# Performance work log

Hardware: AMD Instinct MI355X
Metric: run time of the kernel (lower is better)

Reference implementation:

```python
import jax, jax.numpy as jnp
import numpy as np

E, T, H, I, K = 32, 2048, 1024, 512, 4


def setup_inputs() -> dict:
    key = jax.random.key(0)
    k1, k2, k3, k4, k5 = jax.random.split(key, 5)
    hidden_states = jax.random.normal(k1, (T, H), dtype=jnp.float32)
    top_k_index = jax.random.randint(k2, (T, K), 0, E)
    w = jax.random.uniform(k3, (T, K), dtype=jnp.float32)
    top_k_weights = w / jnp.sum(w, axis=-1, keepdims=True)  # router-like normalized weights
    gate_up_proj = jax.random.normal(k4, (E, 2 * I, H), dtype=jnp.float32) * 0.02
    down_proj = jax.random.normal(k5, (E, H, I), dtype=jnp.float32) * 0.02
    return {
        "hidden_states": hidden_states,
        "top_k_index": top_k_index,
        "top_k_weights": top_k_weights,
        "gate_up_proj": gate_up_proj,
        "down_proj": down_proj,
    }


def reference(hidden_states, top_k_index, top_k_weights, gate_up_proj, down_proj):
    # Faithful to the eager MoE dispatch loop: for each expert e, gather the
    # tokens routed to it, run gate/up/down SwiGLU, scale by routing weight,
    # and scatter-add into the output. Expressed as a scan over experts with a
    # per-token routing weight that is 0 for unrouted tokens (identical math:
    # index_add over (token, slot) pairs == sum_k where(idx==e, w, 0)).
    num_experts = gate_up_proj.shape[0]
    inter = down_proj.shape[2]

    def expert_step(acc, xs):
        gup_w, down_w, e = xs  # [2I, H], [H, I], scalar expert id
        # combined routing weight per token for this expert: [T]
        w_tok = jnp.sum(jnp.where(top_k_index == e, top_k_weights, 0.0), axis=1)
        gu = hidden_states @ gup_w.T              # [T, 2I]
        gate, up = gu[:, :inter], gu[:, inter:]
        h = jax.nn.silu(gate) * up                # [T, I]
        out = h @ down_w.T                        # [T, H]
        return acc + out * w_tok[:, None], None

    init = jnp.zeros_like(hidden_states)
    final_hidden_states, _ = jax.lax.scan(
        expert_step, init,
        (gate_up_proj, down_proj, jnp.arange(num_experts)),
    )
    return final_hidden_states
```

## Files before the change

### kernel.cpp

```cpp
#include <hip/hip_runtime.h>

#define NE 32
#define NT 2048
#define NH 1024
#define NI 512
#define NK 4
#define CAP 512

typedef __attribute__((ext_vector_type(8))) short short8;
typedef __attribute__((ext_vector_type(4))) float floatx4;

static __device__ __forceinline__ unsigned pk_bf16(float x, float y) {
#if __has_builtin(__builtin_amdgcn_cvt_pk_bf16_f32)
    typedef __attribute__((ext_vector_type(2))) __bf16 bf16x2;
    union { bf16x2 v; unsigned u; } c;
    c.v = __builtin_amdgcn_cvt_pk_bf16_f32(x, y);
    return c.u;
#else
    union { float f; unsigned u; } a, b;
    a.f = x; b.f = y;
    unsigned ua = (a.u + 0x7fffu + ((a.u >> 16) & 1u)) >> 16;
    unsigned ub = (b.u + 0x7fffu + ((b.u >> 16) & 1u)) >> 16;
    return (ua & 0xffffu) | (ub << 16);
#endif
}

static __device__ __forceinline__ short8 pack8(const float* p) {
    union { unsigned u[4]; short8 s; } c;
    c.u[0] = pk_bf16(p[0], p[1]);
    c.u[1] = pk_bf16(p[2], p[3]);
    c.u[2] = pk_bf16(p[4], p[5]);
    c.u[3] = pk_bf16(p[6], p[7]);
    return c.s;
}

static __device__ __forceinline__ unsigned short bf16_1(float x) {
    return (unsigned short)(pk_bf16(x, 0.f) & 0xffffu);
}

__global__ void route_kernel(const int* __restrict__ idx,
                             const float* __restrict__ w,
                             int* __restrict__ counts,
                             int* __restrict__ tok,
                             float* __restrict__ wgt) {
    int tid = blockIdx.x * blockDim.x + threadIdx.x;
    if (tid >= NT * NK) return;
    int e = idx[tid];
    int pos = atomicAdd(&counts[e], 1);
    if (pos < CAP) {
        tok[e * CAP + pos] = tid;
        wgt[e * CAP + pos] = w[tid];
    }
}

__global__ void cvt_hidden(const float* __restrict__ hidden,
                           unsigned short* __restrict__ hb16) {
    size_t i = (size_t)(blockIdx.x * 256 + threadIdx.x) * 8;
    float tmp[8];
    *(floatx4*)tmp       = *(const floatx4*)(hidden + i);
    *(floatx4*)(tmp + 4) = *(const floatx4*)(hidden + i + 4);
    *(short8*)(hb16 + i) = pack8(tmp);
}


__global__ __launch_bounds__(256, 2) void gateup_mfma(
    const unsigned short* __restrict__ hb16,
    const float* __restrict__ gup,
    const int* __restrict__ counts,
    const int* __restrict__ tok,
    unsigned short* __restrict__ hbuf)
{
    int e = blockIdx.z;
    int cnt = counts[e]; if (cnt > CAP) cnt = CAP;
    int m0 = blockIdx.y * 128;
    if (m0 >= cnt) return;
    int j0 = blockIdx.x * 64;

    __shared__ __align__(16) short As[2][128][64];
    __shared__ __align__(16) short Bs[2][128][64];

    int tid = threadIdx.x;
    int sr = tid >> 3;
    int sg = tid & 7;

    const unsigned short* aptr[4];
    short* awr[4];
    const float* bptr[4];
    short* bwr[4];
    const float* gup_e = gup + (size_t)e * (2 * NI) * NH;
#pragma unroll
    for (int p = 0; p < 4; p++) {
        int r = p * 32 + sr;
        int mi = m0 + r;
        int tk = tok[e * CAP + (mi < cnt ? mi : m0)];
        aptr[p] = hb16 + (size_t)(tk >> 2) * NH + sg * 8;
        awr[p]  = &As[0][r][(sg ^ (r & 7)) * 8];
        int gj = (r < 64) ? (j0 + r) : (NI + j0 + (r - 64));
        bptr[p] = gup_e + (size_t)gj * NH + sg * 8;
        bwr[p]  = &Bs[0][r][(sg ^ (r & 7)) * 8];
    }

    int wave = tid >> 6, lane = tid & 63;
    int wm = wave >> 1;
    int wj = wave & 1;
    int lcol = lane & 15;
    int quad = lane >> 4;

    floatx4 acc[4][4];
#pragma unroll
    for (int a = 0; a < 4; a++)
#pragma unroll
        for (int b = 0; b < 4; b++) acc[a][b] = (floatx4){0.f, 0.f, 0.f, 0.f};

    short8 ra[4];
    float4 rb[8];
#pragma unroll
    for (int p = 0; p < 4; p++) {
        ra[p] = *(const short8*)(aptr[p]);
        rb[2 * p]     = *(const float4*)(bptr[p]);
        rb[2 * p + 1] = *(const float4*)(bptr[p] + 4);
    }
#pragma unroll
    for (int p = 0; p < 4; p++) {
        *(short8*)(awr[p]) = ra[p];
        union { unsigned u[4]; short8 s; } c;
        c.u[0] = pk_bf16(rb[2 * p].x, rb[2 * p].y);
        c.u[1] = pk_bf16(rb[2 * p].z, rb[2 * p].w);
        c.u[2] = pk_bf16(rb[2 * p + 1].x, rb[2 * p + 1].y);
        c.u[3] = pk_bf16(rb[2 * p + 1].z, rb[2 * p + 1].w);
        *(short8*)(bwr[p]) = c.s;
    }
#pragma unroll
    for (int p = 0; p < 4; p++) {
        ra[p] = *(const short8*)(aptr[p] + 64);
        rb[2 * p]     = *(const float4*)(bptr[p] + 64);
        rb[2 * p + 1] = *(const float4*)(bptr[p] + 68);
    }
    __syncthreads();

    const int NIT = NH / 64;
    for (int it = 0; it < NIT; ++it) {
        int cur = it & 1;
        int co = cur * 8192;
#pragma unroll
        for (int ks = 0; ks < 2; ks++) {
            short8 af[4], bfr[4];
            int q = ks * 4 + quad;
#pragma unroll
            for (int mt = 0; mt < 4; mt++) {
                int R = wm * 64 + mt * 16 + lcol;
                af[mt] = *(const short8*)&As[cur][R][(q ^ (R & 7)) * 8];
            }
#pragma unroll
            for (int nt = 0; nt < 4; nt++) {
                int R = (nt < 2) ? (wj * 32 + nt * 16 + lcol)
                                 : (64 + wj * 32 + (nt - 2) * 16 + lcol);
                bfr[nt] = *(const short8*)&Bs[cur][R][(q ^ (R & 7)) * 8];
            }
#pragma unroll
            for (int mt = 0; mt < 4; mt++)
#pragma unroll
                for (int nt = 0; nt < 4; nt++)
                    acc[mt][nt] = __builtin_amdgcn_mfma_f32_16x16x32_bf16(
                        af[mt], bfr[nt], acc[mt][nt], 0, 0, 0);
        }
        if (it + 1 < NIT) {
            int no = (co ^ 8192);
#pragma unroll
            for (int p = 0; p < 4; p++) {
                *(short8*)(awr[p] + no) = ra[p];
                union { unsigned u[4]; short8 s; } c;
                c.u[0] = pk_bf16(rb[2 * p].x, rb[2 * p].y);
                c.u[1] = pk_bf16(rb[2 * p].z, rb[2 * p].w);
                c.u[2] = pk_bf16(rb[2 * p + 1].x, rb[2 * p + 1].y);
                c.u[3] = pk_bf16(rb[2 * p + 1].z, rb[2 * p + 1].w);
                *(short8*)(bwr[p] + no) = c.s;
            }
            if (it + 2 < NIT) {
                int h2 = (it + 2) * 64;
#pragma unroll
                for (int p = 0; p < 4; p++) {
                    ra[p] = *(const short8*)(aptr[p] + h2);
                    rb[2 * p]     = *(const float4*)(bptr[p] + h2);
                    rb[2 * p + 1] = *(const float4*)(bptr[p] + h2 + 4);
                }
            }
            __syncthreads();
        }
    }

#pragma unroll
    for (int mt = 0; mt < 4; mt++) {
#pragma unroll
        for (int i = 0; i < 4; i++) {
            int m = wm * 64 + mt * 16 + quad * 4 + i;
            if (m0 + m < cnt) {
                int tk = tok[e * CAP + m0 + m];
                unsigned short* hp = hbuf + (size_t)tk * NI + j0 + wj * 32 + lcol;
#pragma unroll
                for (int nt = 0; nt < 2; nt++) {
                    float g = acc[mt][nt][i];
                    float u = acc[mt][nt + 2][i];
                    float h = g / (1.f + __expf(-g)) * u;
                    hp[nt * 16] = bf16_1(h);
                }
            }
        }
    }
}

__global__ __launch_bounds__(256, 2) void down_mfma(
    const unsigned short* __restrict__ hbuf,
    const float* __restrict__ down,
    const int* __restrict__ counts,
    const int* __restrict__ tok,
    const float* __restrict__ wgt,
    float* __restrict__ out)
{
    int e = blockIdx.z;
    int cnt = counts[e]; if (cnt > CAP) cnt = CAP;
    int m0 = blockIdx.y * 128;
    if (m0 >= cnt) return;
    int n0 = blockIdx.x * 128;

    __shared__ __align__(16) short As[2][128][64];
    __shared__ __align__(16) short Bs[2][128][64];

    int tid = threadIdx.x;
    int sr = tid >> 3;
    int sg = tid & 7;

    const unsigned short* aptr[4];
    short* awr[4];
    const float* bptr[4];
    short* bwr[4];
    const float* down_e = down + (size_t)e * NH * NI;
#pragma unroll
    for (int p = 0; p < 4; p++) {
        int r = p * 32 + sr;
        int mi = m0 + r;
        int tk = tok[e * CAP + (mi < cnt ? mi : m0)];
        aptr[p] = hbuf + (size_t)tk * NI + sg * 8;
        awr[p]  = &As[0][r][(sg ^ (r & 7)) * 8];
        bptr[p] = down_e + (size_t)(n0 + r) * NI + sg * 8;
        bwr[p]  = &Bs[0][r][(sg ^ (r & 7)) * 8];
    }

    int wave = tid >> 6, lane = tid & 63;
    int wm = wave >> 1, wn = wave & 1;
    int lcol = lane & 15;
    int quad = lane >> 4;

    floatx4 acc[4][4];
#pragma unroll
    for (int a = 0; a < 4; a++)
#pragma unroll
        for (int b = 0; b < 4; b++) acc[a][b] = (floatx4){0.f, 0.f, 0.f, 0.f};

    short8 ra[4];
    float4 rb[8];
#pragma unroll
    for (int p = 0; p < 4; p++) {
        ra[p] = *(const short8*)(aptr[p]);
        rb[2 * p]     = *(const float4*)(bptr[p]);
        rb[2 * p + 1] = *(const float4*)(bptr[p] + 4);
    }
#pragma unroll
    for (int p = 0; p < 4; p++) {
        *(short8*)(awr[p]) = ra[p];
        union { unsigned u[4]; short8 s; } c;
        c.u[0] = pk_bf16(rb[2 * p].x, rb[2 * p].y);
        c.u[1] = pk_bf16(rb[2 * p].z, rb[2 * p].w);
        c.u[2] = pk_bf16(rb[2 * p + 1].x, rb[2 * p + 1].y);
        c.u[3] = pk_bf16(rb[2 * p + 1].z, rb[2 * p + 1].w);
        *(short8*)(bwr[p]) = c.s;
    }
#pragma unroll
    for (int p = 0; p < 4; p++) {
        ra[p] = *(const short8*)(aptr[p] + 64);
        rb[2 * p]     = *(const float4*)(bptr[p] + 64);
        rb[2 * p + 1] = *(const float4*)(bptr[p] + 68);
    }
    __syncthreads();

    const int NIT = NI / 64;
    for (int it = 0; it < NIT; ++it) {
        int cur = it & 1;
#pragma unroll
        for (int ks = 0; ks < 2; ks++) {
            short8 af[4], bfr[4];
            int q = ks * 4 + quad;
#pragma unroll
            for (int mt = 0; mt < 4; mt++) {
                int R = wm * 64 + mt * 16 + lcol;
                af[mt] = *(const short8*)&As[cur][R][(q ^ (R & 7)) * 8];
            }
#pragma unroll
            for (int nt = 0; nt < 4; nt++) {
                int R = wn * 64 + nt * 16 + lcol;
                bfr[nt] = *(const short8*)&Bs[cur][R][(q ^ (R & 7)) * 8];
            }
#pragma unroll
            for (int mt = 0; mt < 4; mt++)
#pragma unroll
                for (int nt = 0; nt < 4; nt++)
                    acc[mt][nt] = __builtin_amdgcn_mfma_f32_16x16x32_bf16(
                        af[mt], bfr[nt], acc[mt][nt], 0, 0, 0);
        }
        if (it + 1 < NIT) {
            int no = ((cur ^ 1)) * 8192;
#pragma unroll
            for (int p = 0; p < 4; p++) {
                *(short8*)(awr[p] + no) = ra[p];
                union { unsigned u[4]; short8 s; } c;
                c.u[0] = pk_bf16(rb[2 * p].x, rb[2 * p].y);
                c.u[1] = pk_bf16(rb[2 * p].z, rb[2 * p].w);
                c.u[2] = pk_bf16(rb[2 * p + 1].x, rb[2 * p + 1].y);
                c.u[3] = pk_bf16(rb[2 * p + 1].z, rb[2 * p + 1].w);
                *(short8*)(bwr[p] + no) = c.s;
            }
            if (it + 2 < NIT) {
                int i2 = (it + 2) * 64;
#pragma unroll
                for (int p = 0; p < 4; p++) {
                    ra[p] = *(const short8*)(aptr[p] + i2);
                    rb[2 * p]     = *(const float4*)(bptr[p] + i2);
                    rb[2 * p + 1] = *(const float4*)(bptr[p] + i2 + 4);
                }
            }
            __syncthreads();
        }
    }

#pragma unroll
    for (int mt = 0; mt < 4; mt++)
#pragma unroll
        for (int i = 0; i < 4; i++) {
            int m = wm * 64 + mt * 16 + quad * 4 + i;
            if (m0 + m < cnt) {
                int tk = tok[e * CAP + m0 + m];
                float wl = wgt[e * CAP + m0 + m];
                float* op = out + (size_t)(tk >> 2) * NH + n0 + wn * 64 + lcol;
#pragma unroll
                for (int nt = 0; nt < 4; nt++)
                    atomicAdd(op + nt * 16, acc[mt][nt][i] * wl);
            }
        }
}

extern "C" void kernel_launch(void* const* d_in, const int* in_sizes, int n_in,
                              void* d_out, int out_size, void* d_ws, size_t ws_size,
                              hipStream_t stream) {
    const float* hidden = (const float*)d_in[0];
    const int*   tk_idx = (const int*)d_in[1];
    const float* tk_w   = (const float*)d_in[2];
    const float* gup    = (const float*)d_in[3];
    const float* down   = (const float*)d_in[4];
    float* out = (float*)d_out;

    char* ws = (char*)d_ws;
    int*            counts = (int*)ws;
    int*            tok    = (int*)(ws + 256);
    float*          wgt    = (float*)(ws + 256 + NE * CAP * 4);
    unsigned short* hb16   = (unsigned short*)(ws + 256 + 2 * NE * CAP * 4);
    unsigned short* hbuf   = (unsigned short*)(ws + 256 + 2 * NE * CAP * 4
                                               + (size_t)NT * NH * 2);

    hipMemsetAsync(counts, 0, 256, stream);
    hipMemsetAsync(out, 0, (size_t)NT * NH * sizeof(float), stream);

    route_kernel<<<(NT * NK + 255) / 256, 256, 0, stream>>>(tk_idx, tk_w, counts, tok, wgt);
    cvt_hidden<<<(NT * NH / 8) / 256, 256, 0, stream>>>(hidden, hb16);

    dim3 gridG(NI / 64, CAP / 128, NE);
    gateup_mfma<<<gridG, 256, 0, stream>>>(hb16, gup, counts, tok, hbuf);

    dim3 gridD(NH / 128, CAP / 128, NE);
    down_mfma<<<gridD, 256, 0, stream>>>(hbuf, down, counts, tok, wgt, out);
}
```

Measured before the change: 346.0 us.

## Pre-convert expert weights to bf16 and single-buffer LDS tiles in GEMMs

Adds a generic bf16 conversion kernel that converts the gate/up and down weights, as well as the hidden states, into workspace buffers on every call. Both MFMA GEMM kernels then load bf16 weights directly with no per-tile conversion. Their LDS staging drops from double- to single-buffered, with an extra barrier per iteration, and the launch bound rises to 3 blocks per CU. The goal is to remove conversion work and register pressure from the GEMM inner loops and raise occupancy. The cost is a full extra read and write pass over roughly 192MB of fp32 weights per call, plus less overlap between loads and compute.

```diff
diff --git a/kernel.cpp b/kernel.cpp
--- a/kernel.cpp
+++ b/kernel.cpp
@@ -25,15 +25,6 @@
 #endif
 }
 
-static __device__ __forceinline__ short8 pack8(const float* p) {
-    union { unsigned u[4]; short8 s; } c;
-    c.u[0] = pk_bf16(p[0], p[1]);
-    c.u[1] = pk_bf16(p[2], p[3]);
-    c.u[2] = pk_bf16(p[4], p[5]);
-    c.u[3] = pk_bf16(p[6], p[7]);
-    return c.s;
-}
-
 static __device__ __forceinline__ unsigned short bf16_1(float x) {
     return (unsigned short)(pk_bf16(x, 0.f) & 0xffffu);
 }
@@ -53,19 +44,25 @@
     }
 }
 
-__global__ void cvt_hidden(const float* __restrict__ hidden,
-                           unsigned short* __restrict__ hb16) {
-    size_t i = (size_t)(blockIdx.x * 256 + threadIdx.x) * 8;
-    float tmp[8];
-    *(floatx4*)tmp       = *(const floatx4*)(hidden + i);
-    *(floatx4*)(tmp + 4) = *(const floatx4*)(hidden + i + 4);
-    *(short8*)(hb16 + i) = pack8(tmp);
-}
-
-
-__global__ __launch_bounds__(256, 2) void gateup_mfma(
+__global__ void cvt_bf16(const float* __restrict__ src,
+                         unsigned short* __restrict__ dst, int n8) {
+    int i = blockIdx.x * 256 + threadIdx.x;
+    if (i >= n8) return;
+    size_t o = (size_t)i * 8;
+    float4 a = *(const float4*)(src + o);
+    float4 b = *(const float4*)(src + o + 4);
+    union { unsigned u[4]; short8 s; } c;
+    c.u[0] = pk_bf16(a.x, a.y);
+    c.u[1] = pk_bf16(a.z, a.w);
+    c.u[2] = pk_bf16(b.x, b.y);
+    c.u[3] = pk_bf16(b.z, b.w);
+    *(short8*)(dst + o) = c.s;
+}
+
+
+__global__ __launch_bounds__(256, 3) void gateup_mfma(
     const unsigned short* __restrict__ hb16,
-    const float* __restrict__ gup,
+    const unsigned short* __restrict__ gupb,
     const int* __restrict__ counts,
     const int* __restrict__ tok,
     unsigned short* __restrict__ hbuf)
@@ -76,28 +73,28 @@
     if (m0 >= cnt) return;
     int j0 = blockIdx.x * 64;
 
-    __shared__ __align__(16) short As[2][128][64];
-    __shared__ __align__(16) short Bs[2][128][64];
+    __shared__ __align__(16) short As[128][64];
+    __shared__ __align__(16) short Bs[128][64];
 
     int tid = threadIdx.x;
     int sr = tid >> 3;
     int sg = tid & 7;
 
     const unsigned short* aptr[4];
+    const unsigned short* bptr[4];
     short* awr[4];
-    const float* bptr[4];
     short* bwr[4];
-    const float* gup_e = gup + (size_t)e * (2 * NI) * NH;
+    const unsigned short* gup_e = gupb + (size_t)e * (2 * NI) * NH;
 #pragma unroll
     for (int p = 0; p < 4; p++) {
         int r = p * 32 + sr;
         int mi = m0 + r;
         int tk = tok[e * CAP + (mi < cnt ? mi : m0)];
         aptr[p] = hb16 + (size_t)(tk >> 2) * NH + sg * 8;
-        awr[p]  = &As[0][r][(sg ^ (r & 7)) * 8];
+        awr[p]  = &As[r][(sg ^ (r & 7)) * 8];
         int gj = (r < 64) ? (j0 + r) : (NI + j0 + (r - 64));
         bptr[p] = gup_e + (size_t)gj * NH + sg * 8;
-        bwr[p]  = &Bs[0][r][(sg ^ (r & 7)) * 8];
+        bwr[p]  = &Bs[r][(sg ^ (r & 7)) * 8];
     }
 
     int wave = tid >> 6, lane = tid & 63;
@@ -112,36 +109,30 @@
 #pragma unroll
         for (int b = 0; b < 4; b++) acc[a][b] = (floatx4){0.f, 0.f, 0.f, 0.f};
 
-    short8 ra[4];
-    float4 rb[8];
+    short8 ra[4], rbs[4];
 #pragma unroll
     for (int p = 0; p < 4; p++) {
-        ra[p] = *(const short8*)(aptr[p]);
-        rb[2 * p]     = *(const float4*)(bptr[p]);
-        rb[2 * p + 1] = *(const float4*)(bptr[p] + 4);
-    }
-#pragma unroll
-    for (int p = 0; p < 4; p++) {
-        *(short8*)(awr[p]) = ra[p];
-        union { unsigned u[4]; short8 s; } c;
-        c.u[0] = pk_bf16(rb[2 * p].x, rb[2 * p].y);
-        c.u[1] = pk_bf16(rb[2 * p].z, rb[2 * p].w);
-        c.u[2] = pk_bf16(rb[2 * p + 1].x, rb[2 * p + 1].y);
-        c.u[3] = pk_bf16(rb[2 * p + 1].z, rb[2 * p + 1].w);
-        *(short8*)(bwr[p]) = c.s;
-    }
-#pragma unroll
-    for (int p = 0; p < 4; p++) {
-        ra[p] = *(const short8*)(aptr[p] + 64);
-        rb[2 * p]     = *(const float4*)(bptr[p] + 64);
-        rb[2 * p + 1] = *(const float4*)(bptr[p] + 68);
-    }
-    __syncthreads();
+        ra[p]  = *(const short8*)(aptr[p]);
+        rbs[p] = *(const short8*)(bptr[p]);
+    }
 
     const int NIT = NH / 64;
     for (int it = 0; it < NIT; ++it) {
-        int cur = it & 1;
-        int co = cur * 8192;
+        if (it > 0) __syncthreads();
+#pragma unroll
+        for (int p = 0; p < 4; p++) {
+            *(short8*)(awr[p]) = ra[p];
+            *(short8*)(bwr[p]) = rbs[p];
+        }
+        __syncthreads();
+        if (it + 1 < NIT) {
+            int h = (it + 1) * 64;
+#pragma unroll
+            for (int p = 0; p < 4; p++) {
+                ra[p]  = *(const short8*)(aptr[p] + h);
+                rbs[p] = *(const short8*)(bptr[p] + h);
+            }
+        }
 #pragma unroll
         for (int ks = 0; ks < 2; ks++) {
             short8 af[4], bfr[4];
@@ -149,13 +140,13 @@
 #pragma unroll
             for (int mt = 0; mt < 4; mt++) {
                 int R = wm * 64 + mt * 16 + lcol;
-                af[mt] = *(const short8*)&As[cur][R][(q ^ (R & 7)) * 8];
+                af[mt] = *(const short8*)&As[R][(q ^ (R & 7)) * 8];
             }
 #pragma unroll
             for (int nt = 0; nt < 4; nt++) {
                 int R = (nt < 2) ? (wj * 32 + nt * 16 + lcol)
                                  : (64 + wj * 32 + (nt - 2) * 16 + lcol);
-                bfr[nt] = *(const short8*)&Bs[cur][R][(q ^ (R & 7)) * 8];
+                bfr[nt] = *(const short8*)&Bs[R][(q ^ (R & 7)) * 8];
             }
 #pragma unroll
             for (int mt = 0; mt < 4; mt++)
@@ -163,29 +154,6 @@
                 for (int nt = 0; nt < 4; nt++)
                     acc[mt][nt] = __builtin_amdgcn_mfma_f32_16x16x32_bf16(
                         af[mt], bfr[nt], acc[mt][nt], 0, 0, 0);
-        }
-        if (it + 1 < NIT) {
-            int no = (co ^ 8192);
-#pragma unroll
-            for (int p = 0; p < 4; p++) {
-                *(short8*)(awr[p] + no) = ra[p];
-                union { unsigned u[4]; short8 s; } c;
-                c.u[0] = pk_bf16(rb[2 * p].x, rb[2 * p].y);
-                c.u[1] = pk_bf16(rb[2 * p].z, rb[2 * p].w);
-                c.u[2] = pk_bf16(rb[2 * p + 1].x, rb[2 * p + 1].y);
-                c.u[3] = pk_bf16(rb[2 * p + 1].z, rb[2 * p + 1].w);
-                *(short8*)(bwr[p] + no) = c.s;
-            }
-            if (it + 2 < NIT) {
-                int h2 = (it + 2) * 64;
-#pragma unroll
-                for (int p = 0; p < 4; p++) {
-                    ra[p] = *(const short8*)(aptr[p] + h2);
-                    rb[2 * p]     = *(const float4*)(bptr[p] + h2);
-                    rb[2 * p + 1] = *(const float4*)(bptr[p] + h2 + 4);
-                }
-            }
-            __syncthreads();
         }
     }
 
@@ -209,9 +177,9 @@
     }
 }
 
-__global__ __launch_bounds__(256, 2) void down_mfma(
+__global__ __launch_bounds__(256, 3) void down_mfma(
     const unsigned short* __restrict__ hbuf,
-    const float* __restrict__ down,
+    const unsigned short* __restrict__ dwnb,
     const int* __restrict__ counts,
     const int* __restrict__ tok,
     const float* __restrict__ wgt,
@@ -223,27 +191,27 @@
     if (m0 >= cnt) return;
     int n0 = blockIdx.x * 128;
 
-    __shared__ __align__(16) short As[2][128][64];
-    __shared__ __align__(16) short Bs[2][128][64];
+    __shared__ __align__(16) short As[128][64];
+    __shared__ __align__(16) short Bs[128][64];
 
     int tid = threadIdx.x;
     int sr = tid >> 3;
     int sg = tid & 7;
 
     const unsigned short* aptr[4];
+    const unsigned short* bptr[4];
     short* awr[4];
-    const float* bptr[4];
     short* bwr[4];
-    const float* down_e = down + (size_t)e * NH * NI;
+    const unsigned short* dwn_e = dwnb + (size_t)e * NH * NI;
 #pragma unroll
     for (int p = 0; p < 4; p++) {
         int r = p * 32 + sr;
         int mi = m0 + r;
         int tk = tok[e * CAP + (mi < cnt ? mi : m0)];
         aptr[p] = hbuf + (size_t)tk * NI + sg * 8;
-        awr[p]  = &As[0][r][(sg ^ (r & 7)) * 8];
-        bptr[p] = down_e + (size_t)(n0 + r) * NI + sg * 8;
-        bwr[p]  = &Bs[0][r][(sg ^ (r & 7)) * 8];
+        awr[p]  = &As[r][(sg ^ (r & 7)) * 8];
+        bptr[p] = dwn_e + (size_t)(n0 + r) * NI + sg * 8;
+        bwr[p]  = &Bs[r][(sg ^ (r & 7)) * 8];
     }
 
     int wave = tid >> 6, lane = tid & 63;
@@ -257,35 +225,30 @@
 #pragma unroll
         for (int b = 0; b < 4; b++) acc[a][b] = (floatx4){0.f, 0.f, 0.f, 0.f};
 
-    short8 ra[4];
-    float4 rb[8];
+    short8 ra[4], rbs[4];
 #pragma unroll
     for (int p = 0; p < 4; p++) {
-        ra[p] = *(const short8*)(aptr[p]);
-        rb[2 * p]     = *(const float4*)(bptr[p]);
-        rb[2 * p + 1] = *(const float4*)(bptr[p] + 4);
-    }
-#pragma unroll
-    for (int p = 0; p < 4; p++) {
-        *(short8*)(awr[p]) = ra[p];
-        union { unsigned u[4]; short8 s; } c;
-        c.u[0] = pk_bf16(rb[2 * p].x, rb[2 * p].y);
-        c.u[1] = pk_bf16(rb[2 * p].z, rb[2 * p].w);
-        c.u[2] = pk_bf16(rb[2 * p + 1].x, rb[2 * p + 1].y);
-        c.u[3] = pk_bf16(rb[2 * p + 1].z, rb[2 * p + 1].w);
-        *(short8*)(bwr[p]) = c.s;
-    }
-#pragma unroll
-    for (int p = 0; p < 4; p++) {
-        ra[p] = *(const short8*)(aptr[p] + 64);
-        rb[2 * p]     = *(const float4*)(bptr[p] + 64);
-        rb[2 * p + 1] = *(const float4*)(bptr[p] + 68);
-    }
-    __syncthreads();
+        ra[p]  = *(const short8*)(aptr[p]);
+        rbs[p] = *(const short8*)(bptr[p]);
+    }
 
     const int NIT = NI / 64;
     for (int it = 0; it < NIT; ++it) {
-        int cur = it & 1;
+        if (it > 0) __syncthreads();
+#pragma unroll
+        for (int p = 0; p < 4; p++) {
+            *(short8*)(awr[p]) = ra[p];
+            *(short8*)(bwr[p]) = rbs[p];
+        }
+        __syncthreads();
+        if (it + 1 < NIT) {
+            int h = (it + 1) * 64;
+#pragma unroll
+            for (int p = 0; p < 4; p++) {
+                ra[p]  = *(const short8*)(aptr[p] + h);
+                rbs[p] = *(const short8*)(bptr[p] + h);
+            }
+        }
 #pragma unroll
         for (int ks = 0; ks < 2; ks++) {
             short8 af[4], bfr[4];
@@ -293,12 +256,12 @@
 #pragma unroll
             for (int mt = 0; mt < 4; mt++) {
                 int R = wm * 64 + mt * 16 + lcol;
-                af[mt] = *(const short8*)&As[cur][R][(q ^ (R & 7)) * 8];
+                af[mt] = *(const short8*)&As[R][(q ^ (R & 7)) * 8];
             }
 #pragma unroll
             for (int nt = 0; nt < 4; nt++) {
                 int R = wn * 64 + nt * 16 + lcol;
-                bfr[nt] = *(const short8*)&Bs[cur][R][(q ^ (R & 7)) * 8];
+                bfr[nt] = *(const short8*)&Bs[R][(q ^ (R & 7)) * 8];
             }
 #pragma unroll
             for (int mt = 0; mt < 4; mt++)
@@ -306,29 +269,6 @@
                 for (int nt = 0; nt < 4; nt++)
                     acc[mt][nt] = __builtin_amdgcn_mfma_f32_16x16x32_bf16(
                         af[mt], bfr[nt], acc[mt][nt], 0, 0, 0);
-        }
-        if (it + 1 < NIT) {
-            int no = ((cur ^ 1)) * 8192;
-#pragma unroll
-            for (int p = 0; p < 4; p++) {
-                *(short8*)(awr[p] + no) = ra[p];
-                union { unsigned u[4]; short8 s; } c;
-                c.u[0] = pk_bf16(rb[2 * p].x, rb[2 * p].y);
-                c.u[1] = pk_bf16(rb[2 * p].z, rb[2 * p].w);
-                c.u[2] = pk_bf16(rb[2 * p + 1].x, rb[2 * p + 1].y);
-                c.u[3] = pk_bf16(rb[2 * p + 1].z, rb[2 * p + 1].w);
-                *(short8*)(bwr[p] + no) = c.s;
-            }
-            if (it + 2 < NIT) {
-                int i2 = (it + 2) * 64;
-#pragma unroll
-                for (int p = 0; p < 4; p++) {
-                    ra[p] = *(const short8*)(aptr[p] + i2);
-                    rb[2 * p]     = *(const float4*)(bptr[p] + i2);
-                    rb[2 * p + 1] = *(const float4*)(bptr[p] + i2 + 4);
-                }
-            }
-            __syncthreads();
         }
     }
 
@@ -359,22 +299,30 @@
     float* out = (float*)d_out;
 
     char* ws = (char*)d_ws;
-    int*            counts = (int*)ws;
-    int*            tok    = (int*)(ws + 256);
-    float*          wgt    = (float*)(ws + 256 + NE * CAP * 4);
-    unsigned short* hb16   = (unsigned short*)(ws + 256 + 2 * NE * CAP * 4);
-    unsigned short* hbuf   = (unsigned short*)(ws + 256 + 2 * NE * CAP * 4
-                                               + (size_t)NT * NH * 2);
+    size_t off = 0;
+    int*            counts = (int*)(ws + off); off += 256;
+    int*            tok    = (int*)(ws + off); off += (size_t)NE * CAP * 4;
+    float*          wgt    = (float*)(ws + off); off += (size_t)NE * CAP * 4;
+    unsigned short* hb16   = (unsigned short*)(ws + off); off += (size_t)NT * NH * 2;
+    unsigned short* hbuf   = (unsigned short*)(ws + off); off += (size_t)NT * NK * NI * 2;
+    unsigned short* gupb   = (unsigned short*)(ws + off); off += (size_t)NE * 2 * NI * NH * 2;
+    unsigned short* dwnb   = (unsigned short*)(ws + off); off += (size_t)NE * NH * NI * 2;
 
     hipMemsetAsync(counts, 0, 256, stream);
     hipMemsetAsync(out, 0, (size_t)NT * NH * sizeof(float), stream);
 
     route_kernel<<<(NT * NK + 255) / 256, 256, 0, stream>>>(tk_idx, tk_w, counts, tok, wgt);
-    cvt_hidden<<<(NT * NH / 8) / 256, 256, 0, stream>>>(hidden, hb16);
+
+    int n8_h = NT * NH / 8;
+    cvt_bf16<<<(n8_h + 255) / 256, 256, 0, stream>>>(hidden, hb16, n8_h);
+    int n8_g = NE * 2 * NI * NH / 8;
+    cvt_bf16<<<(n8_g + 255) / 256, 256, 0, stream>>>(gup, gupb, n8_g);
+    int n8_d = NE * NH * NI / 8;
+    cvt_bf16<<<(n8_d + 255) / 256, 256, 0, stream>>>(down, dwnb, n8_d);
 
     dim3 gridG(NI / 64, CAP / 128, NE);
-    gateup_mfma<<<gridG, 256, 0, stream>>>(hb16, gup, counts, tok, hbuf);
+    gateup_mfma<<<gridG, 256, 0, stream>>>(hb16, gupb, counts, tok, hbuf);
 
     dim3 gridD(NH / 128, CAP / 128, NE);
-    down_mfma<<<gridD, 256, 0, stream>>>(hbuf, down, counts, tok, wgt, out);
-}
+    down_mfma<<<gridD, 256, 0, stream>>>(hbuf, dwnb, counts, tok, wgt, out);
+}
```

Measured after the change: 370.1 us. 7.0% more time.
